# Kernel optimization log

Hardware: AMD Instinct MI355X
Metric: run time of the kernel (lower is better)

## Reference

```python
import jax, jax.numpy as jnp
import numpy as np
import math

DIM = 256
N = 4096
E = 1024
NEG = -1.0e9


def setup_inputs() -> dict:
    key = jax.random.key(0)
    ks = jax.random.split(key, 10)
    x = jax.random.normal(ks[0], (N, DIM), dtype=jnp.float32)
    # sparse incidence / adjacency (module only uses >0 as mask)
    H = (jax.random.uniform(ks[1], (N, E)) < 0.05).astype(jnp.float32)
    adj = (jax.random.uniform(ks[2], (N, N)) < 0.01).astype(jnp.float32)
    s = 1.0 / math.sqrt(DIM)
    W_he = jax.random.normal(ks[3], (DIM, DIM), dtype=jnp.float32) * s  # HyperedgeAttention.W
    u = jax.random.normal(ks[4], (DIM,), dtype=jnp.float32)            # HyperedgeAttention.u
    W_e = jax.random.normal(ks[5], (DIM, DIM), dtype=jnp.float32) * s  # NodeAttention.W_e
    W_n = jax.random.normal(ks[6], (DIM, DIM), dtype=jnp.float32) * s  # NodeAttention.W_n
    W_g = jax.random.normal(ks[7], (DIM, DIM), dtype=jnp.float32) * s  # GraphAttention.W
    a_g = jax.random.normal(ks[8], (2 * DIM,), dtype=jnp.float32) * s  # GraphAttention.attn weight
    return {"x": x, "H": H, "adj": adj, "W_he": W_he, "u": u,
            "W_e": W_e, "W_n": W_n, "W_g": W_g, "a_g": a_g}


def reference(x, H, adj, W_he, u, W_e, W_n, W_g, a_g):
    n, dim = x.shape
    inv_sqrt_d = 1.0 / math.sqrt(dim)
    maskH = H > 0                       # [N,E] bool
    mask_Hf = maskH.astype(x.dtype)

    # ---- HyperedgeAttention ----
    h_he = x @ W_he                     # [N,dim]
    sc = (h_he @ u) * inv_sqrt_d        # [N]
    scE = jnp.where(maskH, sc[:, None], NEG)      # [N,E]
    A = jax.nn.softmax(scE, axis=0) * mask_Hf     # column softmax over nodes
    e_repr = A.T @ h_he                 # [E,dim]

    # ---- NodeAttention (only B is used) ----
    hn = x @ W_n                        # [N,dim]
    he = e_repr @ W_e                   # [E,dim]
    Bsc = jnp.where(maskH, (hn @ he.T) * inv_sqrt_d, NEG)
    B = jax.nn.softmax(Bsc, axis=1) * mask_Hf     # [N,E]

    # ---- GraphAttention (concat score split: e_ij = lrelu(h_i.a1 + h_j.a2)) ----
    h_g = x @ W_g                       # [N,dim]
    s1 = h_g @ a_g[:dim]                # [N]
    s2 = h_g @ a_g[dim:]                # [N]
    e = jax.nn.leaky_relu(s1[:, None] + s2[None, :], 0.2)   # [N,N]
    maskA = (adj > 0).astype(x.dtype)
    sl = jnp.eye(n, dtype=x.dtype)
    e = e * (maskA + sl) - 1e9 * jnp.clip(1.0 - maskA - sl, 0.0, None)
    G = jax.nn.softmax(e, axis=1)       # [N,N]

    # ---- Mixing ----
    he_sz = jnp.clip(mask_Hf.sum(0), 1.0, None)   # [E]
    M = (G @ mask_Hf) / he_sz[None, :]            # [N,E]
    A_hat = jax.nn.softmax(A.T + M.T, axis=1) * mask_Hf.T   # [E,N]
    e_mix = A_hat @ (x @ W_he)                    # [E,dim]
    B_hat = jax.nn.softmax(B + M, axis=1) * mask_Hf          # [N,E]
    z_h = jax.nn.elu(B_hat @ (e_mix @ W_e))       # [N,dim]
    G_hat = jax.nn.softmax(G + B @ B.T + A @ A.T, axis=1)    # [N,N]
    z_g = jax.nn.elu(G_hat @ (x @ W_g))           # [N,dim]
    return z_h, z_g
```

## Files before the change

kernel.cpp:

```cpp
#include <hip/hip_runtime.h>
#include <math.h>
#include <stdint.h>

#define Nn 4096
#define Ee 1024
#define Dd 256

typedef __attribute__((ext_vector_type(8))) __bf16 bf16x8;
typedef __attribute__((ext_vector_type(4))) float f32x4;
typedef __attribute__((ext_vector_type(8))) unsigned short u16x8;

__device__ __forceinline__ unsigned short f2bf(float f) {
  unsigned int u = __float_as_uint(f);
  unsigned int r = (u + 0x7fffu + ((u >> 16) & 1u)) >> 16;
  return (unsigned short)r;
}
__device__ __forceinline__ float bf2f(unsigned short u) {
  return __uint_as_float(((unsigned int)u) << 16);
}

__device__ __forceinline__ void gload_lds16(const void* g, void* l) {
  __builtin_amdgcn_global_load_lds(
      (__attribute__((address_space(1))) void*)const_cast<void*>(g),
      (__attribute__((address_space(3))) void*)l, 16, 0, 0);
}

__device__ __forceinline__ float block_reduce_sum(float v) {
  __shared__ float sh[4];
  #pragma unroll
  for (int o = 32; o > 0; o >>= 1) v += __shfl_down(v, o);
  int lane = threadIdx.x & 63, w = threadIdx.x >> 6;
  if (lane == 0) sh[w] = v;
  __syncthreads();
  float s = sh[0] + sh[1] + sh[2] + sh[3];
  __syncthreads();
  return s;
}

__global__ __launch_bounds__(256) void gemm_bt_bf16(
    const unsigned short* __restrict__ Ab, const unsigned short* __restrict__ Bb,
    float* __restrict__ Cp, unsigned short* __restrict__ Cb,
    int M, int N, int K, int lda, int ldb, float alpha)
{
  __shared__ unsigned short As[2][128 * 32];
  __shared__ unsigned short Bs[2][128 * 32];
  const int tid = threadIdx.x;
  const int m0 = blockIdx.x * 128, n0 = blockIdx.y * 128;
  const int wave = tid >> 6, lane = tid & 63;
  const int wr = (wave >> 1) * 64, wc = (wave & 1) * 64;
  const int l16 = lane & 15, lq = lane >> 4;
  f32x4 acc[4][4] = {};
  const int NT = K >> 5;

  auto stage = [&](int buf, int kt) {
    const int k0 = kt * 32;
    #pragma unroll
    for (int i = 0; i < 2; ++i) {
      int t2 = tid + i * 256;
      int r = t2 >> 2, c = (t2 & 3) * 8;
      gload_lds16(Ab + (size_t)(m0 + r) * lda + k0 + c, &As[buf][t2 * 8]);
    }
    #pragma unroll
    for (int i = 0; i < 2; ++i) {
      int t2 = tid + i * 256;
      int r = t2 >> 2, c = (t2 & 3) * 8;
      gload_lds16(Bb + (size_t)(n0 + r) * ldb + k0 + c, &Bs[buf][t2 * 8]);
    }
  };

  stage(0, 0);
  __syncthreads();
  int buf = 0;
  for (int kt = 0; kt < NT; ++kt) {
    if (kt + 1 < NT) stage(buf ^ 1, kt + 1);
    bf16x8 af[4], bfr[4];
    #pragma unroll
    for (int m = 0; m < 4; ++m)
      af[m] = *reinterpret_cast<const bf16x8*>(&As[buf][(wr + m * 16 + l16) * 32 + lq * 8]);
    #pragma unroll
    for (int n = 0; n < 4; ++n)
      bfr[n] = *reinterpret_cast<const bf16x8*>(&Bs[buf][(wc + n * 16 + l16) * 32 + lq * 8]);
    #pragma unroll
    for (int m = 0; m < 4; ++m)
      #pragma unroll
      for (int n = 0; n < 4; ++n)
        acc[m][n] = __builtin_amdgcn_mfma_f32_16x16x32_bf16(af[m], bfr[n], acc[m][n], 0, 0, 0);
    __syncthreads();
    buf ^= 1;
  }
  #pragma unroll
  for (int m = 0; m < 4; ++m)
    #pragma unroll
    for (int n = 0; n < 4; ++n) {
      int col = n0 + wc + n * 16 + l16;
      #pragma unroll
      for (int q = 0; q < 4; ++q) {
        int row = m0 + wr + m * 16 + lq * 4 + q;
        size_t idx = (size_t)row * N + col;
        float v = acc[m][n][q] * alpha;
        Cp[idx] = v;
        if (Cb) Cb[idx] = f2bf(v);
      }
    }
}

__global__ __launch_bounds__(256) void gemm_bts_bf16(
    const unsigned short* __restrict__ Ab, const unsigned short* __restrict__ Bb,
    float* __restrict__ Cp, int M, int N, int K, int lda, int ldb, int KS)
{
  __shared__ unsigned short As[2][128 * 32];
  __shared__ unsigned short Bs[2][128 * 32];
  const int tid = threadIdx.x;
  const int m0 = blockIdx.x * 128, n0 = blockIdx.y * 128;
  const int kbase = blockIdx.z * KS;
  const int wave = tid >> 6, lane = tid & 63;
  const int wr = (wave >> 1) * 64, wc = (wave & 1) * 64;
  const int l16 = lane & 15, lq = lane >> 4;
  f32x4 acc[4][4] = {};
  const int NT = KS >> 5;

  auto stage = [&](int buf, int kt) {
    const int k0 = kbase + kt * 32;
    #pragma unroll
    for (int i = 0; i < 2; ++i) {
      int t2 = tid + i * 256;
      int r = t2 >> 2, c = (t2 & 3) * 8;
      gload_lds16(Ab + (size_t)(m0 + r) * lda + k0 + c, &As[buf][t2 * 8]);
    }
    #pragma unroll
    for (int i = 0; i < 2; ++i) {
      int t2 = tid + i * 256;
      int r = t2 >> 2, c = (t2 & 3) * 8;
      gload_lds16(Bb + (size_t)(n0 + r) * ldb + k0 + c, &Bs[buf][t2 * 8]);
    }
  };

  stage(0, 0);
  __syncthreads();
  int buf = 0;
  for (int kt = 0; kt < NT; ++kt) {
    if (kt + 1 < NT) stage(buf ^ 1, kt + 1);
    bf16x8 af[4], bfr[4];
    #pragma unroll
    for (int m = 0; m < 4; ++m)
      af[m] = *reinterpret_cast<const bf16x8*>(&As[buf][(wr + m * 16 + l16) * 32 + lq * 8]);
    #pragma unroll
    for (int n = 0; n < 4; ++n)
      bfr[n] = *reinterpret_cast<const bf16x8*>(&Bs[buf][(wc + n * 16 + l16) * 32 + lq * 8]);
    #pragma unroll
    for (int m = 0; m < 4; ++m)
      #pragma unroll
      for (int n = 0; n < 4; ++n)
        acc[m][n] = __builtin_amdgcn_mfma_f32_16x16x32_bf16(af[m], bfr[n], acc[m][n], 0, 0, 0);
    __syncthreads();
    buf ^= 1;
  }
  #pragma unroll
  for (int m = 0; m < 4; ++m)
    #pragma unroll
    for (int n = 0; n < 4; ++n) {
      int col = n0 + wc + n * 16 + l16;
      #pragma unroll
      for (int q = 0; q < 4; ++q) {
        int row = m0 + wr + m * 16 + lq * 4 + q;
        atomicAdd(&Cp[(size_t)row * N + col], acc[m][n][q]);
      }
    }
}

__global__ __launch_bounds__(256) void gemm_gram_k(
    const unsigned short* __restrict__ CAT,
    unsigned short* __restrict__ Gb,
    float* __restrict__ rowsum)
{
  const int bx = blockIdx.x, by = blockIdx.y;
  if (bx > by) return;
  const int K = 2048;
  __shared__ unsigned short SM[17024];
  unsigned short* Asb = SM;
  unsigned short* Bsb = SM + 8192;
  const int tid = threadIdx.x;
  const int m0 = bx * 128, n0 = by * 128;
  const int wave = tid >> 6, lane = tid & 63;
  const int wr = (wave >> 1) * 64, wc = (wave & 1) * 64;
  const int l16 = lane & 15, lq = lane >> 4;
  f32x4 acc[4][4] = {};
  const int NT = K >> 5;

  auto stage = [&](int buf, int kt) {
    const int k0 = kt * 32;
    #pragma unroll
    for (int i = 0; i < 2; ++i) {
      int t2 = tid + i * 256;
      int r = t2 >> 2, c = (t2 & 3) * 8;
      gload_lds16(CAT + (size_t)(m0 + r) * K + k0 + c, Asb + buf * 4096 + t2 * 8);
    }
    #pragma unroll
    for (int i = 0; i < 2; ++i) {
      int t2 = tid + i * 256;
      int r = t2 >> 2, c = (t2 & 3) * 8;
      gload_lds16(CAT + (size_t)(n0 + r) * K + k0 + c, Bsb + buf * 4096 + t2 * 8);
    }
  };

  stage(0, 0);
  __syncthreads();
  int buf = 0;
  for (int kt = 0; kt < NT; ++kt) {
    if (kt + 1 < NT) stage(buf ^ 1, kt + 1);
    bf16x8 af[4], bfr[4];
    #pragma unroll
    for (int m = 0; m < 4; ++m)
      af[m] = *reinterpret_cast<const bf16x8*>(Asb + buf * 4096 + (wr + m * 16 + l16) * 32 + lq * 8);
    #pragma unroll
    for (int n = 0; n < 4; ++n)
      bfr[n] = *reinterpret_cast<const bf16x8*>(Bsb + buf * 4096 + (wc + n * 16 + l16) * 32 + lq * 8);
    #pragma unroll
    for (int m = 0; m < 4; ++m)
      #pragma unroll
      for (int n = 0; n < 4; ++n)
        acc[m][n] = __builtin_amdgcn_mfma_f32_16x16x32_bf16(af[m], bfr[n], acc[m][n], 0, 0, 0);
    __syncthreads();
    buf ^= 1;
  }
  #pragma unroll
  for (int m = 0; m < 4; ++m)
    #pragma unroll
    for (int q = 0; q < 4; ++q) {
      int row = m0 + wr + m * 16 + lq * 4 + q;
      float s = 0.f;
      #pragma unroll
      for (int n = 0; n < 4; ++n) {
        int col = n0 + wc + n * 16 + l16;
        size_t idx = (size_t)row * Nn + col;
        float e = expf(bf2f(Gb[idx]) + acc[m][n][q]);
        Gb[idx] = f2bf(e);
        s += e;
      }
      s += __shfl_xor(s, 1); s += __shfl_xor(s, 2);
      s += __shfl_xor(s, 4); s += __shfl_xor(s, 8);
      if (l16 == 0) atomicAdd(&rowsum[row], s);
    }
  if (bx == by) return;

  __syncthreads();
  unsigned short* Tg = SM;
  {
    int cc = tid >> 1, r0 = (tid & 1) * 64;
    const unsigned short* src = Gb + (size_t)(n0 + cc) * Nn + m0 + r0;
    unsigned short* dst = Tg + cc * 132 + r0;
    #pragma unroll
    for (int v = 0; v < 8; ++v)
      *reinterpret_cast<u16x8*>(dst + v * 8) = *reinterpret_cast<const u16x8*>(src + v * 8);
  }
  __syncthreads();
  #pragma unroll
  for (int n = 0; n < 4; ++n) {
    int ccl = wc + n * 16 + l16;
    float cs = 0.f;
    #pragma unroll
    for (int m = 0; m < 4; ++m) {
      int sa = ccl * 132 + wr + m * 16 + lq * 4;
      ushort4 lg = *reinterpret_cast<const ushort4*>(&Tg[sa]);
      ushort4 eo;
      float e0 = expf(bf2f(lg.x) + acc[m][n][0]); eo.x = f2bf(e0); cs += e0;
      float e1 = expf(bf2f(lg.y) + acc[m][n][1]); eo.y = f2bf(e1); cs += e1;
      float e2 = expf(bf2f(lg.z) + acc[m][n][2]); eo.z = f2bf(e2); cs += e2;
      float e3 = expf(bf2f(lg.w) + acc[m][n][3]); eo.w = f2bf(e3); cs += e3;
      *reinterpret_cast<ushort4*>(&Tg[sa]) = eo;
    }
    cs += __shfl_xor(cs, 16); cs += __shfl_xor(cs, 32);
    if (lq == 0) atomicAdd(&rowsum[n0 + ccl], cs);
  }
  __syncthreads();
  {
    int cc = tid >> 1, r0 = (tid & 1) * 64;
    const unsigned short* src = Tg + cc * 132 + r0;
    unsigned short* dst = Gb + (size_t)(n0 + cc) * Nn + m0 + r0;
    #pragma unroll
    for (int v = 0; v < 8; ++v)
      *reinterpret_cast<u16x8*>(dst + v * 8) = *reinterpret_cast<const u16x8*>(src + v * 8);
  }
}

__global__ __launch_bounds__(256) void gemm64s_bt_bf16(
    const unsigned short* __restrict__ Ab, const unsigned short* __restrict__ Bb,
    float* __restrict__ Cp, int M, int N, int K, int KS)
{
  __shared__ unsigned short As[2][64 * 64];
  __shared__ unsigned short Bs[2][64 * 64];
  const int tid = threadIdx.x;
  const int m0 = blockIdx.x * 64, n0 = blockIdx.y * 64;
  const int kbase = blockIdx.z * KS;
  const int wave = tid >> 6, lane = tid & 63;
  const int wr = (wave >> 1) * 32, wc = (wave & 1) * 32;
  const int l16 = lane & 15, lq = lane >> 4;
  f32x4 acc[2][2] = {};
  const int NT = KS >> 6;

  auto stage = [&](int buf, int kt) {
    const int k0 = kbase + kt * 64;
    #pragma unroll
    for (int i = 0; i < 2; ++i) {
      int t2 = tid + i * 256;
      int r = t2 >> 3, c = (t2 & 7) * 8;
      gload_lds16(Ab + (size_t)(m0 + r) * K + k0 + c, &As[buf][t2 * 8]);
    }
    #pragma unroll
    for (int i = 0; i < 2; ++i) {
      int t2 = tid + i * 256;
      int r = t2 >> 3, c = (t2 & 7) * 8;
      gload_lds16(Bb + (size_t)(n0 + r) * K + k0 + c, &Bs[buf][t2 * 8]);
    }
  };

  stage(0, 0);
  __syncthreads();
  int buf = 0;
  for (int kt = 0; kt < NT; ++kt) {
    if (kt + 1 < NT) stage(buf ^ 1, kt + 1);
    bf16x8 af[2][2], bfr[2][2];
    #pragma unroll
    for (int m = 0; m < 2; ++m)
      #pragma unroll
      for (int ks = 0; ks < 2; ++ks)
        af[m][ks] = *reinterpret_cast<const bf16x8*>(
            &As[buf][(wr + m * 16 + l16) * 64 + ks * 32 + lq * 8]);
    #pragma unroll
    for (int n = 0; n < 2; ++n)
      #pragma unroll
      for (int ks = 0; ks < 2; ++ks)
        bfr[n][ks] = *reinterpret_cast<const bf16x8*>(
            &Bs[buf][(wc + n * 16 + l16) * 64 + ks * 32 + lq * 8]);
    #pragma unroll
    for (int m = 0; m < 2; ++m)
      #pragma unroll
      for (int n = 0; n < 2; ++n)
        #pragma unroll
        for (int ks = 0; ks < 2; ++ks)
          acc[m][n] = __builtin_amdgcn_mfma_f32_16x16x32_bf16(af[m][ks], bfr[n][ks], acc[m][n], 0, 0, 0);
    __syncthreads();
    buf ^= 1;
  }
  #pragma unroll
  for (int m = 0; m < 2; ++m)
    #pragma unroll
    for (int n = 0; n < 2; ++n) {
      int col = n0 + wc + n * 16 + l16;
      #pragma unroll
      for (int q = 0; q < 4; ++q) {
        int row = m0 + wr + m * 16 + lq * 4 + q;
        atomicAdd(&Cp[(size_t)row * N + col], acc[m][n][q]);
      }
    }
}

__global__ __launch_bounds__(256) void cvt_bf16_k(const float* __restrict__ in,
                                                  unsigned short* __restrict__ out, long n) {
  long i = ((long)blockIdx.x * 256 + threadIdx.x) * 8;
  if (i + 8 > n) return;
  float4 a = *reinterpret_cast<const float4*>(&in[i]);
  float4 b = *reinterpret_cast<const float4*>(&in[i + 4]);
  u16x8 o;
  o[0] = f2bf(a.x); o[1] = f2bf(a.y); o[2] = f2bf(a.z); o[3] = f2bf(a.w);
  o[4] = f2bf(b.x); o[5] = f2bf(b.y); o[6] = f2bf(b.z); o[7] = f2bf(b.w);
  *reinterpret_cast<u16x8*>(&out[i]) = o;
}

__global__ __launch_bounds__(256) void tcvt_k(const float* __restrict__ in,
                                              unsigned short* __restrict__ outT, int R, int S,
                                              const float* __restrict__ coldiv) {
  __shared__ unsigned short tile[64][65];
  int r0 = blockIdx.x * 64, c0 = blockIdx.y * 64;
  int t = threadIdx.x & 63, q = threadIdx.x >> 6;
  float sc = coldiv ? 1.f / fmaxf(coldiv[c0 + t], 1.f) : 1.f;
  for (int rr = q; rr < 64; rr += 4)
    tile[t][rr] = f2bf(in[(long)(r0 + rr) * S + c0 + t] * sc);
  __syncthreads();
  for (int cc = q; cc < 64; cc += 4)
    outT[(long)(c0 + cc) * R + r0 + t] = tile[cc][t];
}

__global__ __launch_bounds__(256) void elu_rows_k(float* __restrict__ p,
                                                  const float* __restrict__ rowsum) {
  long i = ((long)blockIdx.x * 256 + threadIdx.x) * 4;
  float4 v = *reinterpret_cast<const float4*>(&p[i]);
  float sc = 1.f;
  long half = (long)Nn * Dd;
  if (i >= half) sc = 1.f / rowsum[(i - half) >> 8];
  v.x *= sc; v.y *= sc; v.z *= sc; v.w *= sc;
  v.x = v.x > 0.f ? v.x : expm1f(v.x);
  v.y = v.y > 0.f ? v.y : expm1f(v.y);
  v.z = v.z > 0.f ? v.z : expm1f(v.z);
  v.w = v.w > 0.f ? v.w : expm1f(v.w);
  *reinterpret_cast<float4*>(&p[i]) = v;
}

__global__ __launch_bounds__(256) void gemm64_k(
    const float* __restrict__ Ap, const float* __restrict__ Bp, float* __restrict__ Cp,
    unsigned short* __restrict__ Cb,
    int M, int N, int K, int Asm, int Ask, int Bsk, int Bsn)
{
  __shared__ alignas(16) float As[16][68];
  __shared__ alignas(16) float Bs[16][68];
  const int tid = threadIdx.x;
  const int tx = tid & 15, ty = tid >> 4;
  const int m0 = blockIdx.x * 64, n0 = blockIdx.y * 64;
  float acc[4][4] = {};
  for (int k0 = 0; k0 < K; k0 += 16) {
    if (Ask == 1) {
      int mm = tid >> 2, kk = (tid & 3) << 2;
      float4 v = *reinterpret_cast<const float4*>(&Ap[(long)(m0 + mm) * Asm + k0 + kk]);
      As[kk + 0][mm] = v.x; As[kk + 1][mm] = v.y; As[kk + 2][mm] = v.z; As[kk + 3][mm] = v.w;
    } else {
      int kk = tid >> 4, mm = (tid & 15) << 2;
      *reinterpret_cast<float4*>(&As[kk][mm]) =
          *reinterpret_cast<const float4*>(&Ap[(long)(k0 + kk) * Ask + m0 + mm]);
    }
    if (Bsn == 1) {
      int kk = tid >> 4, nn = (tid & 15) << 2;
      *reinterpret_cast<float4*>(&Bs[kk][nn]) =
          *reinterpret_cast<const float4*>(&Bp[(long)(k0 + kk) * Bsk + n0 + nn]);
    } else {
      int nn = tid >> 2, kk = (tid & 3) << 2;
      float4 v = *reinterpret_cast<const float4*>(&Bp[(long)(n0 + nn) * Bsn + k0 + kk]);
      Bs[kk + 0][nn] = v.x; Bs[kk + 1][nn] = v.y; Bs[kk + 2][nn] = v.z; Bs[kk + 3][nn] = v.w;
    }
    __syncthreads();
    #pragma unroll
    for (int kk = 0; kk < 16; ++kk) {
      float4 av = *reinterpret_cast<const float4*>(&As[kk][ty << 2]);
      float4 bv = *reinterpret_cast<const float4*>(&Bs[kk][tx << 2]);
      float a[4] = {av.x, av.y, av.z, av.w};
      float b[4] = {bv.x, bv.y, bv.z, bv.w};
      #pragma unroll
      for (int r = 0; r < 4; ++r)
        #pragma unroll
        for (int c = 0; c < 4; ++c) acc[r][c] = fmaf(a[r], b[c], acc[r][c]);
    }
    __syncthreads();
  }
  #pragma unroll
  for (int r = 0; r < 4; ++r) {
    long base = (long)(m0 + (ty << 2) + r) * N + n0 + (tx << 2);
    float4 o = {acc[r][0], acc[r][1], acc[r][2], acc[r][3]};
    *reinterpret_cast<float4*>(&Cp[base]) = o;
    if (Cb) {
      ushort4 ob = {f2bf(o.x), f2bf(o.y), f2bf(o.z), f2bf(o.w)};
      *reinterpret_cast<ushort4*>(&Cb[base]) = ob;
    }
  }
}

__global__ __launch_bounds__(256) void rowdots_k(
    const float* __restrict__ hcat, const float* __restrict__ u, const float* __restrict__ a_g,
    float* __restrict__ esc, float* __restrict__ s1, float* __restrict__ s2)
{
  int i = blockIdx.x, t = threadIdx.x;
  float hh = hcat[(long)i * 768 + t];
  float hg = hcat[(long)i * 768 + 512 + t];
  float d0 = block_reduce_sum(hh * u[t]);
  float d1 = block_reduce_sum(hg * a_g[t]);
  float d2 = block_reduce_sum(hg * a_g[Dd + t]);
  if (t == 0) {
    esc[i] = expf(d0 * 0.0625f);
    s1[i] = d1;
    s2[i] = d2;
  }
}

__global__ __launch_bounds__(256) void colstats_k(
    const float* __restrict__ H, const float* __restrict__ esc,
    float* __restrict__ colden, float* __restrict__ cnt)
{
  int e = blockIdx.x * 256 + threadIdx.x;
  int r0 = blockIdx.y * 128;
  float d = 0.f, c = 0.f;
  for (int r = r0; r < r0 + 128; ++r) {
    float h = H[(long)r * Ee + e];
    if (h > 0.f) { d += esc[r]; c += 1.f; }
  }
  atomicAdd(&colden[e], d);
  atomicAdd(&cnt[e], c);
}

__global__ __launch_bounds__(256) void fillA_k(
    const float* __restrict__ H, const float* __restrict__ esc,
    const float* __restrict__ colden, float* __restrict__ A,
    unsigned short* __restrict__ CAT, unsigned short* __restrict__ AbT)
{
  __shared__ unsigned short tile[64][68];
  int r0 = blockIdx.x * 64, e0 = blockIdx.y * 64;
  int te = threadIdx.x & 63, tq = threadIdx.x >> 6;
  float cd = colden[e0 + te];
  for (int rr = tq; rr < 64; rr += 4) {
    long idx = (long)(r0 + rr) * Ee + e0 + te;
    float h = H[idx];
    float val = h > 0.f ? esc[r0 + rr] / cd : 0.f;
    A[idx] = val;
    unsigned short vb = f2bf(val);
    CAT[(long)(r0 + rr) * 2048 + 1024 + e0 + te] = vb;
    tile[te][rr] = vb;
  }
  __syncthreads();
  for (int ee = tq; ee < 64; ee += 4)
    AbT[(long)(e0 + ee) * Nn + r0 + te] = tile[ee][te];
}

__global__ __launch_bounds__(256) void brow_k(float* __restrict__ Bbuf,
                                              const float* __restrict__ H,
                                              unsigned short* __restrict__ CAT)
{
  int i = blockIdx.x, t = threadIdx.x;
  long base = (long)i * Ee + t * 4;
  float4 raw = *reinterpret_cast<const float4*>(&Bbuf[base]);
  float4 h = *reinterpret_cast<const float4*>(&H[base]);
  float rr[4] = {raw.x, raw.y, raw.z, raw.w}, hh[4] = {h.x, h.y, h.z, h.w};
  float p[4]; float s = 0.f;
  #pragma unroll
  for (int k = 0; k < 4; ++k) { p[k] = hh[k] > 0.f ? expf(rr[k]) : 0.f; s += p[k]; }
  float den = block_reduce_sum(s);
  float inv = den > 0.f ? 1.f / den : 0.f;
  float4 o = {p[0] * inv, p[1] * inv, p[2] * inv, p[3] * inv};
  *reinterpret_cast<float4*>(&Bbuf[base]) = o;
  ushort4 ob = {f2bf(o.x), f2bf(o.y), f2bf(o.z), f2bf(o.w)};
  *reinterpret_cast<ushort4*>(&CAT[(long)i * 2048 + t * 4]) = ob;
}

__global__ __launch_bounds__(256) void gfill_k(
    const float* __restrict__ adj, const float* __restrict__ s1,
    const float* __restrict__ s2, unsigned short* __restrict__ Gb)
{
  int i = blockIdx.x, t = threadIdx.x;
  float s1i = s1[i];
  float p[16]; float sum = 0.f;
  #pragma unroll
  for (int c = 0; c < 4; ++c) {
    int j = c * 1024 + t * 4;
    float4 a = *reinterpret_cast<const float4*>(&adj[(long)i * Nn + j]);
    float4 sv = *reinterpret_cast<const float4*>(&s2[j]);
    float aa[4] = {a.x, a.y, a.z, a.w}, ss[4] = {sv.x, sv.y, sv.z, sv.w};
    #pragma unroll
    for (int k = 0; k < 4; ++k) {
      float f = (aa[k] > 0.f ? 1.f : 0.f) + ((j + k) == i ? 1.f : 0.f);
      float l = s1i + ss[k];
      l = l > 0.f ? l : 0.2f * l;
      float val = l * f - 1e9f * fmaxf(1.f - f, 0.f);
      float pp = expf(val);
      p[c * 4 + k] = pp; sum += pp;
    }
  }
  float den = block_reduce_sum(sum);
  float inv = 1.f / den;
  #pragma unroll
  for (int c = 0; c < 4; ++c) {
    int j = c * 1024 + t * 4;
    ushort4 ob = {f2bf(p[c * 4] * inv), f2bf(p[c * 4 + 1] * inv),
                  f2bf(p[c * 4 + 2] * inv), f2bf(p[c * 4 + 3] * inv)};
    *reinterpret_cast<ushort4*>(&Gb[(long)i * Nn + j]) = ob;
  }
}

__global__ __launch_bounds__(256) void amstats_k(
    const float* __restrict__ A, const float* __restrict__ Mm, float* __restrict__ aden)
{
  int e = blockIdx.x * 256 + threadIdx.x;
  int r0 = blockIdx.y * 128;
  float d = 0.f;
  for (int r = r0; r < r0 + 128; ++r) {
    long idx = (long)r * Ee + e;
    d += expf(A[idx] + Mm[idx]);
  }
  atomicAdd(&aden[e], d);
}

__global__ __launch_bounds__(256) void ahat_k(
    const float* __restrict__ Abuf, const float* __restrict__ Mm,
    const float* __restrict__ H, const float* __restrict__ aden,
    unsigned short* __restrict__ AhB)
{
  __shared__ float tile[64][65];
  int j0 = blockIdx.x * 64, e0 = blockIdx.y * 64;
  int te = threadIdx.x & 63;
  int tq = threadIdx.x >> 6;
  int e = e0 + te;
  float inv = 1.f / aden[e];
  for (int jj = tq; jj < 64; jj += 4) {
    long idx = (long)(j0 + jj) * Ee + e;
    float val = (H[idx] > 0.f) ? expf(Abuf[idx] + Mm[idx]) * inv : 0.f;
    tile[te][jj] = val;
  }
  __syncthreads();
  for (int ee = tq; ee < 64; ee += 4)
    AhB[(long)(e0 + ee) * Nn + j0 + te] = f2bf(tile[ee][te]);
}

__global__ __launch_bounds__(256) void bhat_k(const float* __restrict__ Bbuf,
                                              const float* __restrict__ Mm,
                                              const float* __restrict__ H,
                                              unsigned short* __restrict__ Bb2)
{
  int i = blockIdx.x, t = threadIdx.x;
  long base = (long)i * Ee + t * 4;
  float4 b = *reinterpret_cast<const float4*>(&Bbuf[base]);
  float4 m = *reinterpret_cast<const float4*>(&Mm[base]);
  float4 h = *reinterpret_cast<const float4*>(&H[base]);
  float bb[4] = {b.x, b.y, b.z, b.w}, mm2[4] = {m.x, m.y, m.z, m.w}, hh[4] = {h.x, h.y, h.z, h.w};
  float p[4]; float s = 0.f;
  #pragma unroll
  for (int k = 0; k < 4; ++k) { p[k] = expf(bb[k] + mm2[k]); s += p[k]; }
  float den = block_reduce_sum(s);
  float inv = 1.f / den;
  #pragma unroll
  for (int k = 0; k < 4; ++k) p[k] = hh[k] > 0.f ? p[k] * inv : 0.f;
  ushort4 ob = {f2bf(p[0]), f2bf(p[1]), f2bf(p[2]), f2bf(p[3])};
  *reinterpret_cast<ushort4*>(&Bb2[base]) = ob;
}

extern "C" void kernel_launch(void* const* d_in, const int* in_sizes, int n_in,
                              void* d_out, int out_size, void* d_ws, size_t ws_size,
                              hipStream_t stream) {
  const float* x    = (const float*)d_in[0];
  const float* H    = (const float*)d_in[1];
  const float* adj  = (const float*)d_in[2];
  const float* W_he = (const float*)d_in[3];
  const float* u    = (const float*)d_in[4];
  const float* W_e  = (const float*)d_in[5];
  const float* W_n  = (const float*)d_in[6];
  const float* W_g  = (const float*)d_in[7];
  const float* a_g  = (const float*)d_in[8];
  float* out = (float*)d_out;
  float* ws  = (float*)d_ws;
  (void)in_sizes; (void)n_in; (void)out_size; (void)ws_size;

  size_t off = 0;
  auto alloc = [&](size_t n) { float* p = ws + off; off += n; return p; };
  float* hcat   = alloc((size_t)Nn * 768);
  float* esc    = alloc(Nn);
  float* s1     = alloc(Nn);
  float* s2     = alloc(Nn);
  float* colden = alloc(Ee);
  float* cnt    = alloc(Ee);
  float* aden   = alloc(Ee);
  float* rowsum = alloc(Nn);
  float* e_repr = alloc((size_t)Ee * Dd);
  float* e_mix  = alloc((size_t)Ee * Dd);
  float* heb    = alloc((size_t)Ee * Dd);
  float* tmp_ew = alloc((size_t)Ee * Dd);
  float* Abuf   = alloc((size_t)Nn * Ee);
  float* Bbuf   = alloc((size_t)Nn * Ee);
  float* Mm     = alloc((size_t)Nn * Ee);
  unsigned short* Gb    = (unsigned short*)alloc((size_t)Nn * Nn / 2);
  unsigned short* CAT   = (unsigned short*)alloc((size_t)Nn * 2048 / 2);
  unsigned short* Hbt   = (unsigned short*)alloc((size_t)Ee * Nn / 2);
  unsigned short* AbT   = (unsigned short*)alloc((size_t)Ee * Nn / 2);
  unsigned short* AhB   = (unsigned short*)alloc((size_t)Ee * Nn / 2);
  unsigned short* hheT  = (unsigned short*)alloc((size_t)Dd * Nn / 2);
  unsigned short* hgT   = (unsigned short*)alloc((size_t)Dd * Nn / 2);
  unsigned short* tewT  = (unsigned short*)alloc((size_t)Dd * Ee / 2);
  unsigned short* Bb2   = (unsigned short*)alloc((size_t)Nn * Ee / 2);
  unsigned short* xb    = (unsigned short*)alloc((size_t)Nn * Dd / 2);
  unsigned short* WcTb  = (unsigned short*)alloc((size_t)768 * Dd / 2);
  unsigned short* hcatB = (unsigned short*)alloc((size_t)Nn * 768 / 2);
  unsigned short* hebB  = (unsigned short*)alloc((size_t)Ee * Dd / 2);

  hipMemsetAsync(colden, 0, (3 * Ee + Nn) * sizeof(float), stream);
  hipMemsetAsync(e_repr, 0, 2 * (size_t)Ee * Dd * sizeof(float), stream);
  hipMemsetAsync(Mm, 0, (size_t)Nn * Ee * sizeof(float), stream);
  hipMemsetAsync(out, 0, 2 * (size_t)Nn * Dd * sizeof(float), stream);

  auto gbt = [&](const unsigned short* A, const unsigned short* B, float* C, unsigned short* Cb,
                 int M, int N, int K, int lda, int ldb, float alpha) {
    gemm_bt_bf16<<<dim3(M / 128, N / 128), 256, 0, stream>>>(A, B, C, Cb, M, N, K, lda, ldb, alpha);
  };
  auto gs64 = [&](const unsigned short* A, const unsigned short* B, float* C,
                  int M, int N, int K, int KS) {
    gemm64s_bt_bf16<<<dim3(M / 64, N / 64, K / KS), 256, 0, stream>>>(A, B, C, M, N, K, KS);
  };
  auto tcvt = [&](const float* in, unsigned short* o, int R, int S, int cols, const float* cd) {
    tcvt_k<<<dim3(R / 64, cols / 64), 256, 0, stream>>>(in, o, R, S, cd);
  };

  cvt_bf16_k<<<(Nn * Dd) / 2048, 256, 0, stream>>>(x, xb, (long)Nn * Dd);
  tcvt(W_he, WcTb, Dd, Dd, Dd, nullptr);
  tcvt(W_n, WcTb + 256 * 256, Dd, Dd, Dd, nullptr);
  tcvt(W_g, WcTb + 2 * 256 * 256, Dd, Dd, Dd, nullptr);
  gbt(xb, WcTb, hcat, hcatB, Nn, 768, Dd, Dd, Dd, 1.f);
  rowdots_k<<<Nn, 256, 0, stream>>>(hcat, u, a_g, esc, s1, s2);
  colstats_k<<<dim3(Ee / 256, 32), 256, 0, stream>>>(H, esc, colden, cnt);
  fillA_k<<<dim3(Nn / 64, Ee / 64), 256, 0, stream>>>(H, esc, colden, Abuf, CAT, AbT);
  tcvt(hcat, hheT, Nn, 768, Dd, nullptr);
  gs64(AbT, hheT, e_repr, Ee, Dd, Nn, 512);
  gemm64_k<<<dim3(Ee / 64, Dd / 64), 256, 0, stream>>>(e_repr, W_e, heb, hebB, Ee, Dd, Dd, Dd, 1, Dd, 1);
  gbt(hcatB + 256, hebB, Bbuf, nullptr, Nn, Ee, Dd, 768, Dd, 0.0625f);
  brow_k<<<Nn, 256, 0, stream>>>(Bbuf, H, CAT);
  gfill_k<<<Nn, 256, 0, stream>>>(adj, s1, s2, Gb);
  tcvt(H, Hbt, Nn, Ee, Ee, cnt);
  gemm_bts_bf16<<<dim3(Nn / 128, Ee / 128, 2), 256, 0, stream>>>(Gb, Hbt, Mm, Nn, Ee, Nn, Nn, Nn, 2048);
  gemm_gram_k<<<dim3(Nn / 128, Nn / 128), 256, 0, stream>>>(CAT, Gb, rowsum);
  amstats_k<<<dim3(Ee / 256, 32), 256, 0, stream>>>(Abuf, Mm, aden);
  ahat_k<<<dim3(Nn / 64, Ee / 64), 256, 0, stream>>>(Abuf, Mm, H, aden, AhB);
  gs64(AhB, hheT, e_mix, Ee, Dd, Nn, 512);
  gemm64_k<<<dim3(Ee / 64, Dd / 64), 256, 0, stream>>>(e_mix, W_e, tmp_ew, nullptr, Ee, Dd, Dd, Dd, 1, Dd, 1);
  bhat_k<<<Nn, 256, 0, stream>>>(Bbuf, Mm, H, Bb2);
  tcvt(tmp_ew, tewT, Ee, Dd, Dd, nullptr);
  gs64(Bb2, tewT, out, Nn, Dd, Ee, 512);
  tcvt(hcat + 512, hgT, Nn, 768, Dd, nullptr);
  gs64(Gb, hgT, out + (size_t)Nn * Dd, Nn, Dd, Nn, 1024);
  elu_rows_k<<<(2 * Nn * Dd) / 1024, 256, 0, stream>>>(out, rowsum);
}
```

Baseline: 618.2 us.

## Fold W_he·W_e into projection GEMM and drop fp32 A/B buffers

Precomputes W_he@W_e and appends it as a fourth projection, so x@(W_he W_e) comes out of the initial GEMM. This removes the two small e_repr@W_e and e_mix@W_e GEMMs and lets e_mix·W_e be produced directly in transposed form. The fp32 A and B matrices are no longer stored; later kernels read the bf16 copies already held in CAT. The Gram kernel now launches only lower-triangle blocks via a linear index instead of early-returning half the grid. The trade-off is extra rounding, since A and B are reread from bf16 and the weight product is reassociated.

```diff
diff --git a/kernel.cpp b/kernel.cpp
--- a/kernel.cpp
+++ b/kernel.cpp
@@ -173,8 +173,11 @@
     unsigned short* __restrict__ Gb,
     float* __restrict__ rowsum)
 {
-  const int bx = blockIdx.x, by = blockIdx.y;
-  if (bx > by) return;
+  int bid = blockIdx.x;
+  int by = (int)((sqrtf(8.f * bid + 1.f) - 1.f) * 0.5f);
+  while ((by + 1) * (by + 2) / 2 <= bid) ++by;
+  while (by * (by + 1) / 2 > bid) --by;
+  int bx = bid - by * (by + 1) / 2;
   const int K = 2048;
   __shared__ unsigned short SM[17024];
   unsigned short* Asb = SM;
@@ -398,7 +401,6 @@
 
 __global__ __launch_bounds__(256) void gemm64_k(
     const float* __restrict__ Ap, const float* __restrict__ Bp, float* __restrict__ Cp,
-    unsigned short* __restrict__ Cb,
     int M, int N, int K, int Asm, int Ask, int Bsk, int Bsn)
 {
   __shared__ alignas(16) float As[16][68];
@@ -445,10 +447,6 @@
     long base = (long)(m0 + (ty << 2) + r) * N + n0 + (tx << 2);
     float4 o = {acc[r][0], acc[r][1], acc[r][2], acc[r][3]};
     *reinterpret_cast<float4*>(&Cp[base]) = o;
-    if (Cb) {
-      ushort4 ob = {f2bf(o.x), f2bf(o.y), f2bf(o.z), f2bf(o.w)};
-      *reinterpret_cast<ushort4*>(&Cb[base]) = ob;
-    }
   }
 }
 
@@ -457,8 +455,8 @@
     float* __restrict__ esc, float* __restrict__ s1, float* __restrict__ s2)
 {
   int i = blockIdx.x, t = threadIdx.x;
-  float hh = hcat[(long)i * 768 + t];
-  float hg = hcat[(long)i * 768 + 512 + t];
+  float hh = hcat[(long)i * 1024 + t];
+  float hg = hcat[(long)i * 1024 + 512 + t];
   float d0 = block_reduce_sum(hh * u[t]);
   float d1 = block_reduce_sum(hg * a_g[t]);
   float d2 = block_reduce_sum(hg * a_g[Dd + t]);
@@ -486,7 +484,7 @@
 
 __global__ __launch_bounds__(256) void fillA_k(
     const float* __restrict__ H, const float* __restrict__ esc,
-    const float* __restrict__ colden, float* __restrict__ A,
+    const float* __restrict__ colden,
     unsigned short* __restrict__ CAT, unsigned short* __restrict__ AbT)
 {
   __shared__ unsigned short tile[64][68];
@@ -497,7 +495,6 @@
     long idx = (long)(r0 + rr) * Ee + e0 + te;
     float h = H[idx];
     float val = h > 0.f ? esc[r0 + rr] / cd : 0.f;
-    A[idx] = val;
     unsigned short vb = f2bf(val);
     CAT[(long)(r0 + rr) * 2048 + 1024 + e0 + te] = vb;
     tile[te][rr] = vb;
@@ -507,7 +504,7 @@
     AbT[(long)(e0 + ee) * Nn + r0 + te] = tile[ee][te];
 }
 
-__global__ __launch_bounds__(256) void brow_k(float* __restrict__ Bbuf,
+__global__ __launch_bounds__(256) void brow_k(const float* __restrict__ Bbuf,
                                               const float* __restrict__ H,
                                               unsigned short* __restrict__ CAT)
 {
@@ -521,9 +518,7 @@
   for (int k = 0; k < 4; ++k) { p[k] = hh[k] > 0.f ? expf(rr[k]) : 0.f; s += p[k]; }
   float den = block_reduce_sum(s);
   float inv = den > 0.f ? 1.f / den : 0.f;
-  float4 o = {p[0] * inv, p[1] * inv, p[2] * inv, p[3] * inv};
-  *reinterpret_cast<float4*>(&Bbuf[base]) = o;
-  ushort4 ob = {f2bf(o.x), f2bf(o.y), f2bf(o.z), f2bf(o.w)};
+  ushort4 ob = {f2bf(p[0] * inv), f2bf(p[1] * inv), f2bf(p[2] * inv), f2bf(p[3] * inv)};
   *reinterpret_cast<ushort4*>(&CAT[(long)i * 2048 + t * 4]) = ob;
 }
 
@@ -562,20 +557,19 @@
 }
 
 __global__ __launch_bounds__(256) void amstats_k(
-    const float* __restrict__ A, const float* __restrict__ Mm, float* __restrict__ aden)
+    const unsigned short* __restrict__ CAT, const float* __restrict__ Mm,
+    float* __restrict__ aden)
 {
   int e = blockIdx.x * 256 + threadIdx.x;
   int r0 = blockIdx.y * 128;
   float d = 0.f;
-  for (int r = r0; r < r0 + 128; ++r) {
-    long idx = (long)r * Ee + e;
-    d += expf(A[idx] + Mm[idx]);
-  }
+  for (int r = r0; r < r0 + 128; ++r)
+    d += expf(bf2f(CAT[(size_t)r * 2048 + 1024 + e]) + Mm[(size_t)r * Ee + e]);
   atomicAdd(&aden[e], d);
 }
 
 __global__ __launch_bounds__(256) void ahat_k(
-    const float* __restrict__ Abuf, const float* __restrict__ Mm,
+    const unsigned short* __restrict__ CAT, const float* __restrict__ Mm,
     const float* __restrict__ H, const float* __restrict__ aden,
     unsigned short* __restrict__ AhB)
 {
@@ -587,7 +581,8 @@
   float inv = 1.f / aden[e];
   for (int jj = tq; jj < 64; jj += 4) {
     long idx = (long)(j0 + jj) * Ee + e;
-    float val = (H[idx] > 0.f) ? expf(Abuf[idx] + Mm[idx]) * inv : 0.f;
+    float a = bf2f(CAT[(size_t)(j0 + jj) * 2048 + 1024 + e]);
+    float val = (H[idx] > 0.f) ? expf(a + Mm[idx]) * inv : 0.f;
     tile[te][jj] = val;
   }
   __syncthreads();
@@ -595,17 +590,18 @@
     AhB[(long)(e0 + ee) * Nn + j0 + te] = f2bf(tile[ee][te]);
 }
 
-__global__ __launch_bounds__(256) void bhat_k(const float* __restrict__ Bbuf,
+__global__ __launch_bounds__(256) void bhat_k(const unsigned short* __restrict__ CAT,
                                               const float* __restrict__ Mm,
                                               const float* __restrict__ H,
                                               unsigned short* __restrict__ Bb2)
 {
   int i = blockIdx.x, t = threadIdx.x;
   long base = (long)i * Ee + t * 4;
-  float4 b = *reinterpret_cast<const float4*>(&Bbuf[base]);
+  ushort4 bu = *reinterpret_cast<const ushort4*>(&CAT[(long)i * 2048 + t * 4]);
   float4 m = *reinterpret_cast<const float4*>(&Mm[base]);
   float4 h = *reinterpret_cast<const float4*>(&H[base]);
-  float bb[4] = {b.x, b.y, b.z, b.w}, mm2[4] = {m.x, m.y, m.z, m.w}, hh[4] = {h.x, h.y, h.z, h.w};
+  float bb[4] = {bf2f(bu.x), bf2f(bu.y), bf2f(bu.z), bf2f(bu.w)};
+  float mm2[4] = {m.x, m.y, m.z, m.w}, hh[4] = {h.x, h.y, h.z, h.w};
   float p[4]; float s = 0.f;
   #pragma unroll
   for (int k = 0; k < 4; ++k) { p[k] = expf(bb[k] + mm2[k]); s += p[k]; }
@@ -635,7 +631,8 @@
 
   size_t off = 0;
   auto alloc = [&](size_t n) { float* p = ws + off; off += n; return p; };
-  float* hcat   = alloc((size_t)Nn * 768);
+  float* hcat4  = alloc((size_t)Nn * 1024);
+  float* Wp     = alloc((size_t)Dd * Dd);
   float* esc    = alloc(Nn);
   float* s1     = alloc(Nn);
   float* s2     = alloc(Nn);
@@ -643,11 +640,8 @@
   float* cnt    = alloc(Ee);
   float* aden   = alloc(Ee);
   float* rowsum = alloc(Nn);
-  float* e_repr = alloc((size_t)Ee * Dd);
-  float* e_mix  = alloc((size_t)Ee * Dd);
   float* heb    = alloc((size_t)Ee * Dd);
-  float* tmp_ew = alloc((size_t)Ee * Dd);
-  float* Abuf   = alloc((size_t)Nn * Ee);
+  float* tewTf  = alloc((size_t)Dd * Ee);
   float* Bbuf   = alloc((size_t)Nn * Ee);
   float* Mm     = alloc((size_t)Nn * Ee);
   unsigned short* Gb    = (unsigned short*)alloc((size_t)Nn * Nn / 2);
@@ -655,17 +649,17 @@
   unsigned short* Hbt   = (unsigned short*)alloc((size_t)Ee * Nn / 2);
   unsigned short* AbT   = (unsigned short*)alloc((size_t)Ee * Nn / 2);
   unsigned short* AhB   = (unsigned short*)alloc((size_t)Ee * Nn / 2);
-  unsigned short* hheT  = (unsigned short*)alloc((size_t)Dd * Nn / 2);
+  unsigned short* hWT   = (unsigned short*)alloc((size_t)Dd * Nn / 2);
   unsigned short* hgT   = (unsigned short*)alloc((size_t)Dd * Nn / 2);
   unsigned short* tewT  = (unsigned short*)alloc((size_t)Dd * Ee / 2);
   unsigned short* Bb2   = (unsigned short*)alloc((size_t)Nn * Ee / 2);
   unsigned short* xb    = (unsigned short*)alloc((size_t)Nn * Dd / 2);
-  unsigned short* WcTb  = (unsigned short*)alloc((size_t)768 * Dd / 2);
-  unsigned short* hcatB = (unsigned short*)alloc((size_t)Nn * 768 / 2);
+  unsigned short* WcTb4 = (unsigned short*)alloc((size_t)1024 * Dd / 2);
+  unsigned short* hcatB = (unsigned short*)alloc((size_t)Nn * 1024 / 2);
   unsigned short* hebB  = (unsigned short*)alloc((size_t)Ee * Dd / 2);
 
   hipMemsetAsync(colden, 0, (3 * Ee + Nn) * sizeof(float), stream);
-  hipMemsetAsync(e_repr, 0, 2 * (size_t)Ee * Dd * sizeof(float), stream);
+  hipMemsetAsync(heb, 0, 2 * (size_t)Ee * Dd * sizeof(float), stream);
   hipMemsetAsync(Mm, 0, (size_t)Nn * Ee * sizeof(float), stream);
   hipMemsetAsync(out, 0, 2 * (size_t)Nn * Dd * sizeof(float), stream);
 
@@ -681,31 +675,32 @@
     tcvt_k<<<dim3(R / 64, cols / 64), 256, 0, stream>>>(in, o, R, S, cd);
   };
 
+  gemm64_k<<<dim3(4, 4), 256, 0, stream>>>(W_he, W_e, Wp, Dd, Dd, Dd, Dd, 1, Dd, 1);
   cvt_bf16_k<<<(Nn * Dd) / 2048, 256, 0, stream>>>(x, xb, (long)Nn * Dd);
-  tcvt(W_he, WcTb, Dd, Dd, Dd, nullptr);
-  tcvt(W_n, WcTb + 256 * 256, Dd, Dd, Dd, nullptr);
-  tcvt(W_g, WcTb + 2 * 256 * 256, Dd, Dd, Dd, nullptr);
-  gbt(xb, WcTb, hcat, hcatB, Nn, 768, Dd, Dd, Dd, 1.f);
-  rowdots_k<<<Nn, 256, 0, stream>>>(hcat, u, a_g, esc, s1, s2);
+  tcvt(W_he, WcTb4, Dd, Dd, Dd, nullptr);
+  tcvt(W_n, WcTb4 + 1 * 256 * 256, Dd, Dd, Dd, nullptr);
+  tcvt(W_g, WcTb4 + 2 * 256 * 256, Dd, Dd, Dd, nullptr);
+  tcvt(Wp, WcTb4 + 3 * 256 * 256, Dd, Dd, Dd, nullptr);
+  gbt(xb, WcTb4, hcat4, hcatB, Nn, 1024, Dd, Dd, Dd, 1.f);
+  rowdots_k<<<Nn, 256, 0, stream>>>(hcat4, u, a_g, esc, s1, s2);
   colstats_k<<<dim3(Ee / 256, 32), 256, 0, stream>>>(H, esc, colden, cnt);
-  fillA_k<<<dim3(Nn / 64, Ee / 64), 256, 0, stream>>>(H, esc, colden, Abuf, CAT, AbT);
-  tcvt(hcat, hheT, Nn, 768, Dd, nullptr);
-  gs64(AbT, hheT, e_repr, Ee, Dd, Nn, 512);
-  gemm64_k<<<dim3(Ee / 64, Dd / 64), 256, 0, stream>>>(e_repr, W_e, heb, hebB, Ee, Dd, Dd, Dd, 1, Dd, 1);
-  gbt(hcatB + 256, hebB, Bbuf, nullptr, Nn, Ee, Dd, 768, Dd, 0.0625f);
+  fillA_k<<<dim3(Nn / 64, Ee / 64), 256, 0, stream>>>(H, esc, colden, CAT, AbT);
+  tcvt(hcat4 + 768, hWT, Nn, 1024, Dd, nullptr);
+  gs64(AbT, hWT, heb, Ee, Dd, Nn, 512);
+  cvt_bf16_k<<<(Ee * Dd) / 2048, 256, 0, stream>>>(heb, hebB, (long)Ee * Dd);
+  gbt(hcatB + 256, hebB, Bbuf, nullptr, Nn, Ee, Dd, 1024, Dd, 0.0625f);
   brow_k<<<Nn, 256, 0, stream>>>(Bbuf, H, CAT);
   gfill_k<<<Nn, 256, 0, stream>>>(adj, s1, s2, Gb);
   tcvt(H, Hbt, Nn, Ee, Ee, cnt);
   gemm_bts_bf16<<<dim3(Nn / 128, Ee / 128, 2), 256, 0, stream>>>(Gb, Hbt, Mm, Nn, Ee, Nn, Nn, Nn, 2048);
-  gemm_gram_k<<<dim3(Nn / 128, Nn / 128), 256, 0, stream>>>(CAT, Gb, rowsum);
-  amstats_k<<<dim3(Ee / 256, 32), 256, 0, stream>>>(Abuf, Mm, aden);
-  ahat_k<<<dim3(Nn / 64, Ee / 64), 256, 0, stream>>>(Abuf, Mm, H, aden, AhB);
-  gs64(AhB, hheT, e_mix, Ee, Dd, Nn, 512);
-  gemm64_k<<<dim3(Ee / 64, Dd / 64), 256, 0, stream>>>(e_mix, W_e, tmp_ew, nullptr, Ee, Dd, Dd, Dd, 1, Dd, 1);
-  bhat_k<<<Nn, 256, 0, stream>>>(Bbuf, Mm, H, Bb2);
-  tcvt(tmp_ew, tewT, Ee, Dd, Dd, nullptr);
+  gemm_gram_k<<<528, 256, 0, stream>>>(CAT, Gb, rowsum);
+  amstats_k<<<dim3(Ee / 256, 32), 256, 0, stream>>>(CAT, Mm, aden);
+  ahat_k<<<dim3(Nn / 64, Ee / 64), 256, 0, stream>>>(CAT, Mm, H, aden, AhB);
+  gs64(hWT, AhB, tewTf, Dd, Ee, Nn, 512);
+  cvt_bf16_k<<<(Dd * Ee) / 2048, 256, 0, stream>>>(tewTf, tewT, (long)Dd * Ee);
+  bhat_k<<<Nn, 256, 0, stream>>>(CAT, Mm, H, Bb2);
   gs64(Bb2, tewT, out, Nn, Dd, Ee, 512);
-  tcvt(hcat + 512, hgT, Nn, 768, Dd, nullptr);
+  tcvt(hcat4 + 512, hgT, Nn, 1024, Dd, nullptr);
   gs64(Gb, hgT, out + (size_t)Nn * Dd, Nn, Dd, Nn, 1024);
   elu_rows_k<<<(2 * Nn * Dd) / 1024, 256, 0, stream>>>(out, rowsum);
 }
```

Result: faster. 587.3 us (-5.0%).
